# Performance work log

Hardware: AMD Instinct MI355X
Metric: run time of the kernel (lower is better)

## Reference

```python
import jax, jax.numpy as jnp
import numpy as np

N = 50000      # nodes (cells)
E = 800000     # directed edges
IN, H1, H2, Z = 512, 128, 128, 64


def setup_inputs() -> dict:
    key = jax.random.key(0)
    ks = jax.random.split(key, 12)
    x = jax.random.normal(ks[0], (N, IN), jnp.float32)
    edge_index = jax.random.randint(ks[1], (2, E), 0, N, dtype=jnp.int64)

    def glorot(k, i, o):
        return jax.random.normal(k, (i, o), jnp.float32) * np.float32(1.0 / np.sqrt(i))

    return {
        "x": x,
        "edge_index": edge_index,
        "W1": glorot(ks[2], IN, H1), "b1": jnp.zeros((H1,), jnp.float32),
        "W2": glorot(ks[3], H1, H2), "b2": jnp.zeros((H2,), jnp.float32),
        "Wm": glorot(ks[4], H2, Z),  "bm": jnp.zeros((Z,), jnp.float32),
        "Ws": glorot(ks[5], H2, Z),  "bs": jnp.zeros((Z,), jnp.float32),
    }


def _gcn_norm(edge_index, n):
    # PyG GCNConv default: add self-loops, sym-normalize D^-1/2 (A+I) D^-1/2
    loops = jnp.arange(n, dtype=edge_index.dtype)
    src = jnp.concatenate([edge_index[0], loops])
    dst = jnp.concatenate([edge_index[1], loops])
    deg = jax.ops.segment_sum(jnp.ones_like(dst, jnp.float32), dst, num_segments=n)
    dis = jnp.where(deg > 0, jax.lax.rsqrt(jnp.maximum(deg, 1.0)), 0.0)
    norm = dis[src] * dis[dst]  # [E+N]
    return src, dst, norm


def _gcn_conv(x, W, b, src, dst, norm, n):
    h = x @ W                          # [N, out] transform first
    msg = h[src] * norm[:, None]       # gather + scale
    out = jax.ops.segment_sum(msg, dst, num_segments=n)  # scatter-add at targets
    return out + b


def reference(x, edge_index, W1, b1, W2, b2, Wm, bm, Ws, bs):
    n = x.shape[0]
    src, dst, norm = _gcn_norm(edge_index, n)
    h = jax.nn.relu(_gcn_conv(x, W1, b1, src, dst, norm, n))
    h = jax.nn.relu(_gcn_conv(h, W2, b2, src, dst, norm, n))
    # dropout p=0.4 is identity in eval mode
    z_mean = _gcn_conv(h, Wm, bm, src, dst, norm, n)
    z_log_std = _gcn_conv(h, Ws, bs, src, dst, norm, n)
    return (z_mean, z_log_std)
```

## Files before the change

kernel.cpp:

```cpp
#include <hip/hip_runtime.h>


using u16 = unsigned short;
typedef __attribute__((ext_vector_type(8))) short short8;
typedef __attribute__((ext_vector_type(4))) float f32x4;

__device__ __forceinline__ void split_bf16(float f, u16& hi, u16& lo) {
    unsigned b = __float_as_uint(f);
    hi = (u16)(b >> 16);
    float rem = f - __uint_as_float(b & 0xFFFF0000u);
    lo = (u16)(__float_as_uint(rem) >> 16);
}

#define TILE_OFF(t) ((t) * 520)

__device__ __forceinline__ int block_mode(const int* __restrict__ ew, int* sflag) {
    if (threadIdx.x == 0) *sflag = 0;
    __syncthreads();
    if (ew[2 * (int)threadIdx.x + 1] != 0) atomicOr(sflag, 1);
    __syncthreads();
    return *sflag ? 0 : 1;
}

__device__ __forceinline__ void gemm_tile(
    const float* __restrict__ A, const u16* __restrict__ Bfh,
    const u16* __restrict__ Bfl, const float* __restrict__ dis,
    float* __restrict__ C, int N, int K, int tile,
    u16* AsH, u16* AsL) {
    const int tid = threadIdx.x;
    const int w = tid >> 6, lane = tid & 63;
    const int m16 = lane & 15, quad = lane >> 4;
    const int row0 = tile * 64;

    const int s_ar = w * 16 + (lane & 15);
    const int s_ak = (lane >> 4) * 8;
    const int a_dst = TILE_OFF(w) + lane * 8;

    const int R = (w >> 1) * 32, Cc = (w & 1) * 64;
    const int atile = (w >> 1) * 2;
    const int btile = (w & 1) * 4;

    const int ksteps = K >> 5;
    const u16* bfh = Bfh + ((size_t)btile * ksteps) * 512 + lane * 8;
    const u16* bfl = Bfl + ((size_t)btile * ksteps) * 512 + lane * 8;

    f32x4 acc[2][4];
#pragma unroll
    for (int i = 0; i < 2; ++i)
#pragma unroll
        for (int j = 0; j < 4; ++j) acc[i][j] = (f32x4)0.f;

    float dr[2][4];
#pragma unroll
    for (int i = 0; i < 2; ++i)
#pragma unroll
        for (int r = 0; r < 4; ++r) {
            int gr = row0 + R + i * 16 + quad * 4 + r;
            dr[i][r] = dis[gr < N ? gr : N - 1];
        }

    const int grow = row0 + s_ar;
    const bool ok = (grow < N);
    const float* aptr = A + (size_t)grow * K + s_ak;

    float av[8];
    {
        f32x4 v0 = (f32x4)0.f, v1 = (f32x4)0.f;
        if (ok) { v0 = *(const f32x4*)&aptr[0]; v1 = *(const f32x4*)&aptr[4]; }
#pragma unroll
        for (int q = 0; q < 4; ++q) { av[q] = v0[q]; av[4 + q] = v1[q]; }
    }

    for (int ks = 0; ks < ksteps; ++ks) {
        short8 fbh[4], fbl[4];
#pragma unroll
        for (int j = 0; j < 4; ++j) {
            fbh[j] = *(const short8*)(bfh + (size_t)(j * ksteps + ks) * 512);
            fbl[j] = *(const short8*)(bfl + (size_t)(j * ksteps + ks) * 512);
        }

        short8 ah, al;
#pragma unroll
        for (int q = 0; q < 8; ++q) {
            u16 h, l;
            split_bf16(av[q], h, l);
            ah[q] = (short)h;
            al[q] = (short)l;
        }
        __syncthreads();
        *(short8*)&AsH[a_dst] = ah;
        *(short8*)&AsL[a_dst] = al;
        __syncthreads();

        if (ks + 1 < ksteps) {
            const int k0 = (ks + 1) * 32;
            f32x4 v0 = (f32x4)0.f, v1 = (f32x4)0.f;
            if (ok) { v0 = *(const f32x4*)&aptr[k0]; v1 = *(const f32x4*)&aptr[k0 + 4]; }
#pragma unroll
            for (int q = 0; q < 4; ++q) { av[q] = v0[q]; av[4 + q] = v1[q]; }
        }

        short8 fah[2], fal[2];
#pragma unroll
        for (int i = 0; i < 2; ++i) {
            fah[i] = *(const short8*)&AsH[TILE_OFF(atile + i) + lane * 8];
            fal[i] = *(const short8*)&AsL[TILE_OFF(atile + i) + lane * 8];
        }

#pragma unroll
        for (int i = 0; i < 2; ++i)
#pragma unroll
            for (int j = 0; j < 4; ++j) {
                acc[i][j] = __builtin_amdgcn_mfma_f32_16x16x32_bf16(
                    fah[i], fbh[j], acc[i][j], 0, 0, 0);
                acc[i][j] = __builtin_amdgcn_mfma_f32_16x16x32_bf16(
                    fah[i], fbl[j], acc[i][j], 0, 0, 0);
                acc[i][j] = __builtin_amdgcn_mfma_f32_16x16x32_bf16(
                    fal[i], fbh[j], acc[i][j], 0, 0, 0);
            }
    }

#pragma unroll
    for (int i = 0; i < 2; ++i) {
#pragma unroll
        for (int r = 0; r < 4; ++r) {
            int gr = row0 + R + i * 16 + quad * 4 + r;
            if (gr < N) {
#pragma unroll
                for (int j = 0; j < 4; ++j)
                    C[(size_t)gr * 128 + Cc + j * 16 + m16] = acc[i][j][r] * dr[i][r];
            }
        }
    }
}

__global__ void conv_deg_kernel(
    const float* __restrict__ W1, const float* __restrict__ W2,
    const float* __restrict__ Wm, const float* __restrict__ Ws,
    u16* __restrict__ B1h, u16* __restrict__ B1l,
    u16* __restrict__ B2h, u16* __restrict__ B2l,
    u16* __restrict__ Bch, u16* __restrict__ Bcl,
    const int* __restrict__ ew, int* __restrict__ deg, int E) {
    __shared__ int sflag;
    int mode = block_mode(ew, &sflag);
    int gtid = blockIdx.x * 256 + threadIdx.x;
    if (gtid < 98304) {
        int idx = gtid;
        u16 h, l;
        if (idx < 65536) {
            int t = idx >> 13, ks = (idx >> 9) & 15, L = (idx >> 3) & 63, q = idx & 7;
            int col = t * 16 + (L & 15);
            int k = ks * 32 + (L >> 4) * 8 + q;
            split_bf16(W1[k * 128 + col], h, l);
            B1h[idx] = h; B1l[idx] = l;
        } else if (idx < 81920) {
            int o = idx - 65536;
            int t = o >> 11, ks = (o >> 9) & 3, L = (o >> 3) & 63, q = o & 7;
            int col = t * 16 + (L & 15);
            int k = ks * 32 + (L >> 4) * 8 + q;
            split_bf16(W2[k * 128 + col], h, l);
            B2h[o] = h; B2l[o] = l;
        } else {
            int o = idx - 81920;
            int t = o >> 11, ks = (o >> 9) & 3, L = (o >> 3) & 63, q = o & 7;
            int col = t * 16 + (L & 15);
            int k = ks * 32 + (L >> 4) * 8 + q;
            float f = (col < 64) ? Wm[k * 64 + col] : Ws[k * 64 + (col - 64)];
            split_bf16(f, h, l);
            Bch[o] = h; Bcl[o] = l;
        }
    }
    if (gtid < E) {
        int d = mode ? ew[2 * E + 2 * gtid] : ew[E + gtid];
        atomicAdd(&deg[d], 1);
    }
}

__global__ void scan_block_kernel(const int* __restrict__ deg, int* __restrict__ rowptr,
                                  int* __restrict__ aux, float* __restrict__ dis, int N) {
    __shared__ int s[256];
    int i = blockIdx.x * 256 + threadIdx.x;
    int v = (i < N) ? deg[i] : 0;
    if (i < N) dis[i] = rsqrtf((float)v + 1.0f);
    s[threadIdx.x] = v;
    __syncthreads();
    for (int off = 1; off < 256; off <<= 1) {
        int t = (threadIdx.x >= off) ? s[threadIdx.x - off] : 0;
        __syncthreads();
        s[threadIdx.x] += t;
        __syncthreads();
    }
    if (i < N) rowptr[i] = s[threadIdx.x] - v;
    if (threadIdx.x == 255) aux[blockIdx.x] = s[255];
}

__global__ void offsets_kernel(int* __restrict__ rowptr, const int* __restrict__ aux,
                               int* __restrict__ cursor, int N, int E, int nch) {
    __shared__ int s[256];
    const int b = blockIdx.x, tid = threadIdx.x;
    int v = (tid < nch) ? aux[tid] : 0;
    s[tid] = v;
    __syncthreads();
    for (int off = 1; off < 256; off <<= 1) {
        int t = (tid >= off) ? s[tid - off] : 0;
        __syncthreads();
        s[tid] += t;
        __syncthreads();
    }
    const int excl = (b == 0) ? 0 : s[b - 1];
    int i = b * 256 + tid;
    if (i < N) {
        int rp = rowptr[i] + excl;
        rowptr[i] = rp;
        cursor[i] = rp;
    }
    if (b == 0 && tid == 0) rowptr[N] = E;
}

__global__ __launch_bounds__(256) void gemm1_fill_kernel(
    const float* __restrict__ A, const u16* __restrict__ Bfh,
    const u16* __restrict__ Bfl, const float* __restrict__ dis,
    float* __restrict__ C, int N, int gtiles,
    const int* __restrict__ ew, int* __restrict__ cursor,
    int* __restrict__ csr_src, int E) {
    __shared__ __align__(16) u16 AsH[4 * 520], AsL[4 * 520];
    __shared__ int sflag;
    if ((int)blockIdx.x < gtiles) {
        gemm_tile(A, Bfh, Bfl, dis, C, N, 512, blockIdx.x, AsH, AsL);
    } else {
        int mode = block_mode(ew, &sflag);
        int e = ((int)blockIdx.x - gtiles) * 256 + (int)threadIdx.x;
        if (e < E) {
            int s = mode ? ew[2 * e] : ew[e];
            int d = mode ? ew[2 * E + 2 * e] : ew[E + e];
            int pos = atomicAdd(&cursor[d], 1);
            csr_src[pos] = s;
        }
    }
}

__global__ __launch_bounds__(256) void gemm_mfma(const float* __restrict__ A,
                                                 const u16* __restrict__ Bfh,
                                                 const u16* __restrict__ Bfl,
                                                 const float* __restrict__ dis,
                                                 float* __restrict__ C,
                                                 int N, int K) {
    __shared__ __align__(16) u16 AsH[4 * 520], AsL[4 * 520];
    gemm_tile(A, Bfh, Bfl, dis, C, N, K, blockIdx.x, AsH, AsL);
}

__global__ __launch_bounds__(256) void propagate_kernel(
    const float* __restrict__ hs, const int* __restrict__ rowptr,
    const int* __restrict__ csr_src, const float* __restrict__ dis,
    const float* __restrict__ bias, float* __restrict__ out, int N, int do_relu) {
    int wave = (blockIdx.x * 256 + threadIdx.x) >> 6;
    int lane = threadIdx.x & 63;
    if (wave >= N) return;
    const int v = wave;
    const int half = lane >> 5, c = lane & 31;
    const int f4 = c * 4;
    const float dv = dis[v];
    f32x4 acc = (f32x4)0.f;
    const int beg = rowptr[v], end = rowptr[v + 1];
    int i = beg;
    for (; i + 8 <= end; i += 8) {
        int s[4];
        f32x4 g[4];
#pragma unroll
        for (int u = 0; u < 4; ++u) s[u] = csr_src[i + 2 * u + half];
#pragma unroll
        for (int u = 0; u < 4; ++u) g[u] = *(const f32x4*)&hs[(size_t)s[u] * 128 + f4];
#pragma unroll
        for (int u = 0; u < 4; ++u) acc += g[u];
    }
    for (; i + 2 <= end; i += 2) {
        int s = csr_src[i + half];
        acc += *(const f32x4*)&hs[(size_t)s * 128 + f4];
    }
    if (i < end && half == 0) {
        int s = csr_src[i];
        acc += *(const f32x4*)&hs[(size_t)s * 128 + f4];
    }
#pragma unroll
    for (int k = 0; k < 4; ++k) acc[k] += __shfl_xor(acc[k], 32);
    if (half == 0) {
        const f32x4 hv = *(const f32x4*)&hs[(size_t)v * 128 + f4];
        const f32x4 b = *(const f32x4*)&bias[f4];
        f32x4 o;
#pragma unroll
        for (int k = 0; k < 4; ++k) {
            float t = dv * (acc[k] + hv[k]) + b[k];
            o[k] = do_relu ? fmaxf(t, 0.f) : t;
        }
        *(f32x4*)&out[(size_t)v * 128 + f4] = o;
    }
}

__global__ void __launch_bounds__(256) propagate_final_kernel(
    const float* __restrict__ hs, const int* __restrict__ rowptr,
    const int* __restrict__ csr_src, const float* __restrict__ dis,
    const float* __restrict__ bm, const float* __restrict__ bs,
    float* __restrict__ out, int N) {
    int wave = (blockIdx.x * 256 + threadIdx.x) >> 6;
    int lane = threadIdx.x & 63;
    if (wave >= N) return;
    const int v = wave;
    const int half = lane >> 5, c = lane & 31;
    const int f4 = c * 4;
    const float dv = dis[v];
    f32x4 acc = (f32x4)0.f;
    const int beg = rowptr[v], end = rowptr[v + 1];
    int i = beg;
    for (; i + 8 <= end; i += 8) {
        int s[4];
        f32x4 g[4];
#pragma unroll
        for (int u = 0; u < 4; ++u) s[u] = csr_src[i + 2 * u + half];
#pragma unroll
        for (int u = 0; u < 4; ++u) g[u] = *(const f32x4*)&hs[(size_t)s[u] * 128 + f4];
#pragma unroll
        for (int u = 0; u < 4; ++u) acc += g[u];
    }
    for (; i + 2 <= end; i += 2) {
        int s = csr_src[i + half];
        acc += *(const f32x4*)&hs[(size_t)s * 128 + f4];
    }
    if (i < end && half == 0) {
        int s = csr_src[i];
        acc += *(const f32x4*)&hs[(size_t)s * 128 + f4];
    }
#pragma unroll
    for (int k = 0; k < 4; ++k) acc[k] += __shfl_xor(acc[k], 32);
    if (half == 0) {
        const f32x4 hv = *(const f32x4*)&hs[(size_t)v * 128 + f4];
        f32x4 o;
        if (f4 < 64) {
            const f32x4 b = *(const f32x4*)&bm[f4];
#pragma unroll
            for (int k = 0; k < 4; ++k) o[k] = dv * (acc[k] + hv[k]) + b[k];
            *(f32x4*)&out[(size_t)v * 64 + f4] = o;
        } else {
            const int g = f4 - 64;
            const f32x4 b = *(const f32x4*)&bs[g];
#pragma unroll
            for (int k = 0; k < 4; ++k) o[k] = dv * (acc[k] + hv[k]) + b[k];
            *(f32x4*)&out[(size_t)N * 64 + (size_t)v * 64 + g] = o;
        }
    }
}

extern "C" void kernel_launch(void* const* d_in, const int* in_sizes, int n_in,
                              void* d_out, int out_size, void* d_ws, size_t ws_size,
                              hipStream_t stream) {
    const float* x  = (const float*)d_in[0];
    const int*   ew = (const int*)d_in[1];
    const float* W1 = (const float*)d_in[2];
    const float* b1 = (const float*)d_in[3];
    const float* W2 = (const float*)d_in[4];
    const float* b2 = (const float*)d_in[5];
    const float* Wm = (const float*)d_in[6];
    const float* bm = (const float*)d_in[7];
    const float* Ws = (const float*)d_in[8];
    const float* bs = (const float*)d_in[9];
    float* out = (float*)d_out;

    const int IN = 512, H = 128;
    const int N = in_sizes[0] / IN;
    const int E = in_sizes[1] / 2;

    char* base = (char*)d_ws;
    size_t off = 0;
    auto alloc = [&](size_t bytes) -> char* {
        char* p = base + off;
        off = (off + bytes + 255) & ~(size_t)255;
        return p;
    };
    int*   deg     = (int*)  alloc((size_t)N * 4);
    int*   cursor  = (int*)  alloc((size_t)N * 4);
    float* dis     = (float*)alloc((size_t)N * 4);
    int*   rowptr  = (int*)  alloc((size_t)(N + 1) * 4);
    int*   aux     = (int*)  alloc(256 * 4);
    int*   csr_src = (int*)  alloc((size_t)E * 4);
    u16*   B1h     = (u16*)  alloc((size_t)IN * H * 2);
    u16*   B1l     = (u16*)  alloc((size_t)IN * H * 2);
    u16*   B2h     = (u16*)  alloc((size_t)H * H * 2);
    u16*   B2l     = (u16*)  alloc((size_t)H * H * 2);
    u16*   Bch     = (u16*)  alloc((size_t)H * H * 2);
    u16*   Bcl     = (u16*)  alloc((size_t)H * H * 2);
    float* hA      = (float*)alloc((size_t)N * H * 4);
    float* hB      = (float*)alloc((size_t)N * H * 4);
    (void)ws_size; (void)n_in; (void)out_size;

    hipMemsetAsync(deg, 0, (size_t)N * 4, stream);

    const int eblocks = (E + 255) / 256;
    const int nblocks = (N + 255) / 256;
    const int nch = nblocks;
    const int gtiles = (N + 63) / 64;
    const int pblocks = (N * 64 + 255) / 256;

    conv_deg_kernel<<<eblocks, 256, 0, stream>>>(
        W1, W2, Wm, Ws, B1h, B1l, B2h, B2l, Bch, Bcl, ew, deg, E);
    scan_block_kernel<<<nblocks, 256, 0, stream>>>(deg, rowptr, aux, dis, N);
    offsets_kernel<<<nblocks, 256, 0, stream>>>(rowptr, aux, cursor, N, E, nch);
    gemm1_fill_kernel<<<gtiles + eblocks, 256, 0, stream>>>(
        x, B1h, B1l, dis, hA, N, gtiles, ew, cursor, csr_src, E);
    propagate_kernel<<<pblocks, 256, 0, stream>>>(hA, rowptr, csr_src, dis,
                                                  b1, hB, N, 1);
    gemm_mfma<<<gtiles, 256, 0, stream>>>(hB, B2h, B2l, dis, hA, N, H);
    propagate_kernel<<<pblocks, 256, 0, stream>>>(hA, rowptr, csr_src, dis,
                                                  b2, hB, N, 1);
    gemm_mfma<<<gtiles, 256, 0, stream>>>(hB, Bch, Bcl, dis, hA, N, H);
    propagate_final_kernel<<<pblocks, 256, 0, stream>>>(hA, rowptr, csr_src, dis,
                                                        bm, bs, out, N);
}
```

Baseline: 451.8 us.

## Split first-layer GEMM over K into two halves with atomic accumulation

The 512-deep first GEMM is split into two K-halves, each handled by its own block, which doubles the number of GEMM blocks and shortens each block's serial K loop. Partial results are combined with float atomic adds into the output buffer. That buffer is now zeroed inside the offsets kernel beforehand. The change adds an extra full pass of writes over the buffer plus atomic traffic, and the summation order becomes nondeterministic.

```diff
diff --git a/kernel.cpp b/kernel.cpp
--- a/kernel.cpp
+++ b/kernel.cpp
@@ -25,8 +25,8 @@
 __device__ __forceinline__ void gemm_tile(
     const float* __restrict__ A, const u16* __restrict__ Bfh,
     const u16* __restrict__ Bfl, const float* __restrict__ dis,
-    float* __restrict__ C, int N, int K, int tile,
-    u16* AsH, u16* AsL) {
+    float* __restrict__ C, int N, int K, int tile, int kb, int ke,
+    int atomic, u16* AsH, u16* AsL) {
     const int tid = threadIdx.x;
     const int w = tid >> 6, lane = tid & 63;
     const int m16 = lane & 15, quad = lane >> 4;
@@ -65,13 +65,14 @@
 
     float av[8];
     {
+        const int k0 = kb * 32;
         f32x4 v0 = (f32x4)0.f, v1 = (f32x4)0.f;
-        if (ok) { v0 = *(const f32x4*)&aptr[0]; v1 = *(const f32x4*)&aptr[4]; }
+        if (ok) { v0 = *(const f32x4*)&aptr[k0]; v1 = *(const f32x4*)&aptr[k0 + 4]; }
 #pragma unroll
         for (int q = 0; q < 4; ++q) { av[q] = v0[q]; av[4 + q] = v1[q]; }
     }
 
-    for (int ks = 0; ks < ksteps; ++ks) {
+    for (int ks = kb; ks < ke; ++ks) {
         short8 fbh[4], fbl[4];
 #pragma unroll
         for (int j = 0; j < 4; ++j) {
@@ -92,7 +93,7 @@
         *(short8*)&AsL[a_dst] = al;
         __syncthreads();
 
-        if (ks + 1 < ksteps) {
+        if (ks + 1 < ke) {
             const int k0 = (ks + 1) * 32;
             f32x4 v0 = (f32x4)0.f, v1 = (f32x4)0.f;
             if (ok) { v0 = *(const f32x4*)&aptr[k0]; v1 = *(const f32x4*)&aptr[k0 + 4]; }
@@ -126,9 +127,17 @@
         for (int r = 0; r < 4; ++r) {
             int gr = row0 + R + i * 16 + quad * 4 + r;
             if (gr < N) {
-#pragma unroll
-                for (int j = 0; j < 4; ++j)
-                    C[(size_t)gr * 128 + Cc + j * 16 + m16] = acc[i][j][r] * dr[i][r];
+                if (atomic) {
+#pragma unroll
+                    for (int j = 0; j < 4; ++j)
+                        unsafeAtomicAdd(&C[(size_t)gr * 128 + Cc + j * 16 + m16],
+                                        acc[i][j][r] * dr[i][r]);
+                } else {
+#pragma unroll
+                    for (int j = 0; j < 4; ++j)
+                        C[(size_t)gr * 128 + Cc + j * 16 + m16] =
+                            acc[i][j][r] * dr[i][r];
+                }
             }
         }
     }
@@ -195,7 +204,8 @@
 }
 
 __global__ void offsets_kernel(int* __restrict__ rowptr, const int* __restrict__ aux,
-                               int* __restrict__ cursor, int N, int E, int nch) {
+                               int* __restrict__ cursor, float* __restrict__ hA,
+                               int N, int E, int nch) {
     __shared__ int s[256];
     const int b = blockIdx.x, tid = threadIdx.x;
     int v = (tid < nch) ? aux[tid] : 0;
@@ -215,21 +225,29 @@
         cursor[i] = rp;
     }
     if (b == 0 && tid == 0) rowptr[N] = E;
+    f32x4* hz = (f32x4*)hA;
+    const size_t nvec = (size_t)N * 32;
+    const size_t step = (size_t)gridDim.x * 256;
+    for (size_t z = (size_t)b * 256 + tid; z < nvec; z += step)
+        hz[z] = (f32x4)0.f;
 }
 
 __global__ __launch_bounds__(256) void gemm1_fill_kernel(
     const float* __restrict__ A, const u16* __restrict__ Bfh,
     const u16* __restrict__ Bfl, const float* __restrict__ dis,
-    float* __restrict__ C, int N, int gtiles,
+    float* __restrict__ C, int N, int gtiles2,
     const int* __restrict__ ew, int* __restrict__ cursor,
     int* __restrict__ csr_src, int E) {
     __shared__ __align__(16) u16 AsH[4 * 520], AsL[4 * 520];
     __shared__ int sflag;
-    if ((int)blockIdx.x < gtiles) {
-        gemm_tile(A, Bfh, Bfl, dis, C, N, 512, blockIdx.x, AsH, AsL);
+    if ((int)blockIdx.x < gtiles2) {
+        const int t = blockIdx.x >> 1;
+        const int kh = blockIdx.x & 1;
+        gemm_tile(A, Bfh, Bfl, dis, C, N, 512, t, kh * 8, kh * 8 + 8, 1,
+                  AsH, AsL);
     } else {
         int mode = block_mode(ew, &sflag);
-        int e = ((int)blockIdx.x - gtiles) * 256 + (int)threadIdx.x;
+        int e = ((int)blockIdx.x - gtiles2) * 256 + (int)threadIdx.x;
         if (e < E) {
             int s = mode ? ew[2 * e] : ew[e];
             int d = mode ? ew[2 * E + 2 * e] : ew[E + e];
@@ -246,7 +264,7 @@
                                                  float* __restrict__ C,
                                                  int N, int K) {
     __shared__ __align__(16) u16 AsH[4 * 520], AsL[4 * 520];
-    gemm_tile(A, Bfh, Bfl, dis, C, N, K, blockIdx.x, AsH, AsL);
+    gemm_tile(A, Bfh, Bfl, dis, C, N, K, blockIdx.x, 0, K >> 5, 0, AsH, AsL);
 }
 
 __global__ __launch_bounds__(256) void propagate_kernel(
@@ -391,7 +409,7 @@
     float* hB      = (float*)alloc((size_t)N * H * 4);
     (void)ws_size; (void)n_in; (void)out_size;
 
-    hipMemsetAsync(deg, 0, (size_t)N * 4, stream);
+    (void)hipMemsetAsync(deg, 0, (size_t)N * 4, stream);
 
     const int eblocks = (E + 255) / 256;
     const int nblocks = (N + 255) / 256;
@@ -402,9 +420,9 @@
     conv_deg_kernel<<<eblocks, 256, 0, stream>>>(
         W1, W2, Wm, Ws, B1h, B1l, B2h, B2l, Bch, Bcl, ew, deg, E);
     scan_block_kernel<<<nblocks, 256, 0, stream>>>(deg, rowptr, aux, dis, N);
-    offsets_kernel<<<nblocks, 256, 0, stream>>>(rowptr, aux, cursor, N, E, nch);
-    gemm1_fill_kernel<<<gtiles + eblocks, 256, 0, stream>>>(
-        x, B1h, B1l, dis, hA, N, gtiles, ew, cursor, csr_src, E);
+    offsets_kernel<<<nblocks, 256, 0, stream>>>(rowptr, aux, cursor, hA, N, E, nch);
+    gemm1_fill_kernel<<<2 * gtiles + eblocks, 256, 0, stream>>>(
+        x, B1h, B1l, dis, hA, N, 2 * gtiles, ew, cursor, csr_src, E);
     propagate_kernel<<<pblocks, 256, 0, stream>>>(hA, rowptr, csr_src, dis,
                                                   b1, hB, N, 1);
     gemm_mfma<<<gtiles, 256, 0, stream>>>(hB, B2h, B2l, dis, hA, N, H);
```

Result: slower. 501.0 us (+10.9%).
